# Kernel tuning notes

Measured on AMD Instinct MI355X. Metric: run time of the kernel, lower is better.

## Reference

```python
import jax, jax.numpy as jnp
import numpy as np

B, N, D_MODEL, LAP = 64, 64, 256, 16


def setup_inputs() -> dict:
    key = jax.random.key(0)
    ks = jax.random.split(key, 8)
    adj = jax.random.randint(ks[0], (B, N, N), 0, 2, dtype=jnp.int32)
    node_feats = jax.random.normal(ks[1], (B, N, D_MODEL), dtype=jnp.float32)
    eigvec = jax.random.normal(ks[2], (B, N, LAP), dtype=jnp.float32)
    W_lap = jax.random.normal(ks[3], (LAP, D_MODEL), dtype=jnp.float32) / np.sqrt(LAP)
    W_edge = jax.random.normal(ks[4], (1 + 2 * LAP, D_MODEL), dtype=jnp.float32) / np.sqrt(1 + 2 * LAP)
    b_edge = jax.random.normal(ks[5], (D_MODEL,), dtype=jnp.float32) * 0.02
    type_embed = jax.random.normal(ks[6], (2, D_MODEL), dtype=jnp.float32)
    graph_tok = jax.random.normal(ks[7], (1, 1, D_MODEL), dtype=jnp.float32)
    return {"adj": adj, "node_feats": node_feats, "eigvec": eigvec,
            "W_lap": W_lap, "W_edge": W_edge, "b_edge": b_edge,
            "type_embed": type_embed, "graph_tok": graph_tok}


def reference(adj, node_feats, eigvec, W_lap, W_edge, b_edge, type_embed, graph_tok):
    b, n, _ = adj.shape
    d = graph_tok.shape[-1]
    # node tokens: feats + LapPE projection
    node_tok = node_feats + jnp.einsum('bnl,ld->bnd', eigvec, W_lap)
    # upper-triangular candidate edges (fixed M = n(n-1)/2, jit-friendly)
    iu, ju = jnp.triu_indices(n, k=1)               # [M]
    valid = adj[:, iu, ju] > 0                       # [B, M]
    # stable compaction: valid edges first (matches torch per-graph extraction order)
    order = jnp.argsort(~valid, axis=1, stable=True) # [B, M]
    src = iu[order]                                  # [B, M]
    dst = ju[order]
    valid_sorted = jnp.take_along_axis(valid, order, axis=1)
    Pu = jnp.take_along_axis(eigvec, src[..., None], axis=1)  # [B, M, LAP]
    Pv = jnp.take_along_axis(eigvec, dst[..., None], axis=1)
    m = src.shape[1]
    edge_in = jnp.concatenate([jnp.ones((b, m, 1), eigvec.dtype), Pu, Pv], axis=-1)
    etok = jnp.einsum('bmf,fd->bmd', edge_in, W_edge) + b_edge + type_embed[1]
    etok = jnp.where(valid_sorted[..., None], etok, 0.0)      # zeros at padding
    pad_mask_edges = ~valid_sorted                             # True = padding
    gtok = jnp.broadcast_to(graph_tok, (b, 1, d))
    seq_embeds = jnp.concatenate([gtok, node_tok, etok], axis=1)  # [B, 1+n+M, d]
    pad_mask = jnp.concatenate([jnp.zeros((b, 1 + n), bool), pad_mask_edges], axis=1)
    return seq_embeds, pad_mask
```

## Files before the change

### kernel.cpp

```cpp
#include <hip/hip_runtime.h>

#define B_ 64
#define N_ 64
#define D_ 256
#define LAP_ 16
#define M_ 2016
#define TOK_ 2081

__global__ __launch_bounds__(256) void compact_kernel(const int* __restrict__ adj,
                                                      int* __restrict__ pack) {
    int b = blockIdx.x;
    int t = threadIdx.x;
    __shared__ int s[256];
    __shared__ int s_total;

    int ii[8], jj[8], vv[8];
    int c = 0;
#pragma unroll
    for (int k = 0; k < 8; k++) {
        int m = t * 8 + k;
        int valid = 0, i = 0, j = 0;
        if (m < M_) {
            float fm = (float)m;
            int gi = (int)((127.0f - sqrtf(127.0f * 127.0f - 8.0f * fm)) * 0.5f);
            if (gi < 0) gi = 0;
            if (gi > 62) gi = 62;
            while (gi > 0 && (127 * gi - gi * gi) / 2 > m) gi--;
            while (gi < 62 && (127 * (gi + 1) - (gi + 1) * (gi + 1)) / 2 <= m) gi++;
            i = gi;
            j = i + 1 + (m - (127 * i - i * i) / 2);
            valid = (adj[b * (N_ * N_) + i * N_ + j] > 0) ? 1 : 0;
        }
        ii[k] = i; jj[k] = j; vv[k] = valid;
        c += valid;
    }
    s[t] = c;
    __syncthreads();
    for (int off = 1; off < 256; off <<= 1) {
        int v = (t >= off) ? s[t - off] : 0;
        __syncthreads();
        s[t] += v;
        __syncthreads();
    }
    if (t == 255) s_total = s[255];
    __syncthreads();
    int total = s_total;
    int run = s[t] - c;
#pragma unroll
    for (int k = 0; k < 8; k++) {
        int m = t * 8 + k;
        if (m < M_) {
            int p;
            if (vv[k]) { p = run; run++; }
            else       { p = total + (m - run); }
            pack[b * M_ + p] = ii[k] | (jj[k] << 8) | (vv[k] << 16);
        }
    }
}

__global__ __launch_bounds__(256) void node_kernel(const float* __restrict__ node_feats,
                                                   const float* __restrict__ eigvec,
                                                   const float* __restrict__ W_lap,
                                                   const float* __restrict__ graph_tok,
                                                   float* __restrict__ out) {
    int b = blockIdx.x;
    int t = threadIdx.x;
    int n = blockIdx.y * 4 + (t >> 6);
    int lane = t & 63;
    const float* e = eigvec + (size_t)(b * N_ + n) * LAP_;
    float4 acc = ((const float4*)(node_feats + ((size_t)b * N_ + n) * D_))[lane];
#pragma unroll
    for (int l = 0; l < LAP_; l++) {
        float el = e[l];
        float4 w = ((const float4*)(W_lap + l * D_))[lane];
        acc.x += el * w.x; acc.y += el * w.y; acc.z += el * w.z; acc.w += el * w.w;
    }
    ((float4*)(out + (size_t)b * TOK_ * D_ + (size_t)(1 + n) * D_))[lane] = acc;

    if (blockIdx.y == 0) {
        out[(size_t)b * TOK_ * D_ + t] = graph_tok[t];
        float* mask = out + (size_t)B_ * TOK_ * D_;
        if (t < 1 + N_) mask[b * TOK_ + t] = 0.0f;
    }
}

__global__ __launch_bounds__(256) void edge_kernel(const float* __restrict__ eigvec,
                                                   const float* __restrict__ W_edge,
                                                   const float* __restrict__ b_edge,
                                                   const float* __restrict__ type_embed,
                                                   const int* __restrict__ pack,
                                                   float* __restrict__ out) {
    __shared__ float sEig[N_ * LAP_];

    int b = blockIdx.x;
    int t = threadIdx.x;
    int wave = t >> 6, lane = t & 63;

    ((float4*)sEig)[t] = ((const float4*)(eigvec + (size_t)b * N_ * LAP_))[t];

    float4 base = ((const float4*)W_edge)[lane];
    {
        float4 bb = ((const float4*)b_edge)[lane];
        float4 te = ((const float4*)(type_embed + D_))[lane];
        base.x += bb.x + te.x; base.y += bb.y + te.y;
        base.z += bb.z + te.z; base.w += bb.w + te.w;
    }
    float4 w1[LAP_], w2[LAP_];
#pragma unroll
    for (int l = 0; l < LAP_; l++) {
        w1[l] = ((const float4*)(W_edge + (1 + l) * D_))[lane];
        w2[l] = ((const float4*)(W_edge + (1 + LAP_ + l) * D_))[lane];
    }
    __syncthreads();

    float* maskb = out + (size_t)B_ * TOK_ * D_ + (size_t)b * TOK_ + 1 + N_;
    float* outb = out + (size_t)b * TOK_ * D_ + (size_t)(1 + N_) * D_;

#pragma unroll
    for (int k = 0; k < 8; k++) {
        int p = blockIdx.y * 32 + wave * 8 + k;
        int pk = pack[b * M_ + p];
        float4 acc = make_float4(0.f, 0.f, 0.f, 0.f);
        int valid = (pk >> 16) & 1;
        if (valid) {
            int si = pk & 0xff, di = (pk >> 8) & 0xff;
            const float4* eu4 = (const float4*)(sEig + si * LAP_);
            const float4* ev4 = (const float4*)(sEig + di * LAP_);
            float4 eu[4], ev[4];
#pragma unroll
            for (int q = 0; q < 4; q++) { eu[q] = eu4[q]; ev[q] = ev4[q]; }
            acc = base;
            const float* euf = (const float*)eu;
            const float* evf = (const float*)ev;
#pragma unroll
            for (int l = 0; l < LAP_; l++) {
                float pu = euf[l], pv = evf[l];
                acc.x += pu * w1[l].x + pv * w2[l].x;
                acc.y += pu * w1[l].y + pv * w2[l].y;
                acc.z += pu * w1[l].z + pv * w2[l].z;
                acc.w += pu * w1[l].w + pv * w2[l].w;
            }
        }
        ((float4*)(outb + (size_t)p * D_))[lane] = acc;
        if (lane == 0) maskb[p] = valid ? 0.0f : 1.0f;
    }
}

extern "C" void kernel_launch(void* const* d_in, const int* in_sizes, int n_in,
                              void* d_out, int out_size, void* d_ws, size_t ws_size,
                              hipStream_t stream) {
    const int*   adj        = (const int*)d_in[0];
    const float* node_feats = (const float*)d_in[1];
    const float* eigvec     = (const float*)d_in[2];
    const float* W_lap      = (const float*)d_in[3];
    const float* W_edge     = (const float*)d_in[4];
    const float* b_edge     = (const float*)d_in[5];
    const float* type_embed = (const float*)d_in[6];
    const float* graph_tok  = (const float*)d_in[7];
    float* out = (float*)d_out;
    int* pack = (int*)d_ws;

    compact_kernel<<<dim3(B_), dim3(256), 0, stream>>>(adj, pack);
    node_kernel<<<dim3(B_, 16), dim3(256), 0, stream>>>(node_feats, eigvec, W_lap,
                                                        graph_tok, out);
    edge_kernel<<<dim3(B_, 63), dim3(256), 0, stream>>>(eigvec, W_edge, b_edge,
                                                        type_embed, pack, out);
}
```

Baseline: 179.9 us.

## Fuse compaction, node and edge kernels into one launch with per-block ballot compaction

```diff
diff --git a/kernel.cpp b/kernel.cpp
--- a/kernel.cpp
+++ b/kernel.cpp
@@ -7,142 +7,171 @@
 #define M_ 2016
 #define TOK_ 2081
 
-__global__ __launch_bounds__(256) void compact_kernel(const int* __restrict__ adj,
-                                                      int* __restrict__ pack) {
-    int b = blockIdx.x;
-    int t = threadIdx.x;
-    __shared__ int s[256];
-    __shared__ int s_total;
+typedef float v4f __attribute__((ext_vector_type(4)));
+typedef float v2f __attribute__((ext_vector_type(2)));
 
-    int ii[8], jj[8], vv[8];
-    int c = 0;
-#pragma unroll
-    for (int k = 0; k < 8; k++) {
-        int m = t * 8 + k;
-        int valid = 0, i = 0, j = 0;
-        if (m < M_) {
-            float fm = (float)m;
-            int gi = (int)((127.0f - sqrtf(127.0f * 127.0f - 8.0f * fm)) * 0.5f);
-            if (gi < 0) gi = 0;
-            if (gi > 62) gi = 62;
-            while (gi > 0 && (127 * gi - gi * gi) / 2 > m) gi--;
-            while (gi < 62 && (127 * (gi + 1) - (gi + 1) * (gi + 1)) / 2 <= m) gi++;
-            i = gi;
-            j = i + 1 + (m - (127 * i - i * i) / 2);
-            valid = (adj[b * (N_ * N_) + i * N_ + j] > 0) ? 1 : 0;
-        }
-        ii[k] = i; jj[k] = j; vv[k] = valid;
-        c += valid;
-    }
-    s[t] = c;
-    __syncthreads();
-    for (int off = 1; off < 256; off <<= 1) {
-        int v = (t >= off) ? s[t - off] : 0;
-        __syncthreads();
-        s[t] += v;
-        __syncthreads();
-    }
-    if (t == 255) s_total = s[255];
-    __syncthreads();
-    int total = s_total;
-    int run = s[t] - c;
-#pragma unroll
-    for (int k = 0; k < 8; k++) {
-        int m = t * 8 + k;
-        if (m < M_) {
-            int p;
-            if (vv[k]) { p = run; run++; }
-            else       { p = total + (m - run); }
-            pack[b * M_ + p] = ii[k] | (jj[k] << 8) | (vv[k] << 16);
-        }
-    }
+__device__ __forceinline__ void ij_from_m(int m, int& i, int& j) {
+    float fm = (float)m;
+    int gi = (int)((127.0f - sqrtf(127.0f * 127.0f - 8.0f * fm)) * 0.5f);
+    if (gi < 0) gi = 0;
+    if (gi > 62) gi = 62;
+    while (gi > 0 && (127 * gi - gi * gi) / 2 > m) gi--;
+    while (gi < 62 && (127 * (gi + 1) - (gi + 1) * (gi + 1)) / 2 <= m) gi++;
+    i = gi;
+    j = gi + 1 + (m - (127 * gi - gi * gi) / 2);
 }
 
-__global__ __launch_bounds__(256) void node_kernel(const float* __restrict__ node_feats,
-                                                   const float* __restrict__ eigvec,
-                                                   const float* __restrict__ W_lap,
-                                                   const float* __restrict__ graph_tok,
-                                                   float* __restrict__ out) {
-    int b = blockIdx.x;
-    int t = threadIdx.x;
-    int n = blockIdx.y * 4 + (t >> 6);
-    int lane = t & 63;
-    const float* e = eigvec + (size_t)(b * N_ + n) * LAP_;
-    float4 acc = ((const float4*)(node_feats + ((size_t)b * N_ + n) * D_))[lane];
-#pragma unroll
-    for (int l = 0; l < LAP_; l++) {
-        float el = e[l];
-        float4 w = ((const float4*)(W_lap + l * D_))[lane];
-        acc.x += el * w.x; acc.y += el * w.y; acc.z += el * w.z; acc.w += el * w.w;
-    }
-    ((float4*)(out + (size_t)b * TOK_ * D_ + (size_t)(1 + n) * D_))[lane] = acc;
+__global__ __launch_bounds__(256, 4) void fused_kernel(
+    const int*   __restrict__ adj,
+    const float* __restrict__ node_feats,
+    const float* __restrict__ eigvec,
+    const float* __restrict__ W_lap,
+    const float* __restrict__ W_edge,
+    const float* __restrict__ b_edge,
+    const float* __restrict__ type_embed,
+    const float* __restrict__ graph_tok,
+    float*       __restrict__ out)
+{
+    __shared__ float sEig[N_ * LAP_];
+    __shared__ unsigned long long sWords[32];
+    __shared__ int sPref[32];
+    __shared__ int sTok[32];
+    __shared__ int sTotal;
 
-    if (blockIdx.y == 0) {
-        out[(size_t)b * TOK_ * D_ + t] = graph_tok[t];
-        float* mask = out + (size_t)B_ * TOK_ * D_;
-        if (t < 1 + N_) mask[b * TOK_ + t] = 0.0f;
-    }
-}
-
-__global__ __launch_bounds__(256) void edge_kernel(const float* __restrict__ eigvec,
-                                                   const float* __restrict__ W_edge,
-                                                   const float* __restrict__ b_edge,
-                                                   const float* __restrict__ type_embed,
-                                                   const int* __restrict__ pack,
-                                                   float* __restrict__ out) {
-    __shared__ float sEig[N_ * LAP_];
-
-    int b = blockIdx.x;
-    int t = threadIdx.x;
-    int wave = t >> 6, lane = t & 63;
+    const int b = blockIdx.x;
+    const int y = blockIdx.y;
+    const int t = threadIdx.x;
+    const int wave = t >> 6, lane = t & 63;
 
     ((float4*)sEig)[t] = ((const float4*)(eigvec + (size_t)b * N_ * LAP_))[t];
 
-    float4 base = ((const float4*)W_edge)[lane];
-    {
-        float4 bb = ((const float4*)b_edge)[lane];
-        float4 te = ((const float4*)(type_embed + D_))[lane];
-        base.x += bb.x + te.x; base.y += bb.y + te.y;
-        base.z += bb.z + te.z; base.w += bb.w + te.w;
+    if (y == 63) {
+        float4 wl[LAP_];
+#pragma unroll
+        for (int l = 0; l < LAP_; l++)
+            wl[l] = ((const float4*)(W_lap + l * D_))[lane];
+        __syncthreads();
+        float* outB = out + (size_t)b * TOK_ * D_;
+#pragma unroll 2
+        for (int it = 0; it < 16; it++) {
+            int n = it * 4 + wave;
+            float4 a = ((const float4*)(node_feats + ((size_t)b * N_ + n) * D_))[lane];
+            const float* e = sEig + n * LAP_;
+#pragma unroll
+            for (int l = 0; l < LAP_; l++) {
+                float el = e[l];
+                a.x += el * wl[l].x; a.y += el * wl[l].y;
+                a.z += el * wl[l].z; a.w += el * wl[l].w;
+            }
+            __builtin_nontemporal_store(*(const v4f*)&a,
+                (v4f*)(outB + (size_t)(1 + n) * D_) + lane);
+        }
+        outB[t] = graph_tok[t];
+        if (t < 1 + N_)
+            out[(size_t)B_ * TOK_ * D_ + (size_t)b * TOK_ + t] = 0.0f;
+        return;
     }
-    float4 w1[LAP_], w2[LAP_];
+
+#pragma unroll
+    for (int k = 0; k < 8; k++) {
+        int m = k * 256 + t;
+        int valid = 0;
+        if (m < M_) {
+            int i, j;
+            ij_from_m(m, i, j);
+            valid = (adj[b * (N_ * N_) + i * N_ + j] > 0) ? 1 : 0;
+        }
+        unsigned long long blt = __ballot(valid);
+        if (lane == 0) sWords[k * 4 + wave] = blt;
+    }
+
+    const int h = wave & 1;
+    const int cbase = h * 128 + lane * 2;
+    float2 base2;
+    base2.x = W_edge[cbase]     + b_edge[cbase]     + type_embed[D_ + cbase];
+    base2.y = W_edge[cbase + 1] + b_edge[cbase + 1] + type_embed[D_ + cbase + 1];
+    float2 w1[LAP_], w2[LAP_];
 #pragma unroll
     for (int l = 0; l < LAP_; l++) {
-        w1[l] = ((const float4*)(W_edge + (1 + l) * D_))[lane];
-        w2[l] = ((const float4*)(W_edge + (1 + LAP_ + l) * D_))[lane];
+        w1[l] = *(const float2*)(W_edge + (1 + l) * D_ + cbase);
+        w2[l] = *(const float2*)(W_edge + (1 + LAP_ + l) * D_ + cbase);
     }
     __syncthreads();
 
-    float* maskb = out + (size_t)B_ * TOK_ * D_ + (size_t)b * TOK_ + 1 + N_;
-    float* outb = out + (size_t)b * TOK_ * D_ + (size_t)(1 + N_) * D_;
+    if (t < 32) {
+        int c = __popcll(sWords[t]);
+        int inc = c;
+#pragma unroll
+        for (int off = 1; off < 32; off <<= 1) {
+            int v = __shfl_up(inc, off);
+            if (lane >= off) inc += v;
+        }
+        sPref[t] = inc - c;
+        if (t == 31) sTotal = inc;
+    }
+    __syncthreads();
 
-#pragma unroll
-    for (int k = 0; k < 8; k++) {
-        int p = blockIdx.y * 32 + wave * 8 + k;
-        int pk = pack[b * M_ + p];
-        float4 acc = make_float4(0.f, 0.f, 0.f, 0.f);
-        int valid = (pk >> 16) & 1;
-        if (valid) {
-            int si = pk & 0xff, di = (pk >> 8) & 0xff;
+    const int total = sTotal;
+    if (t < 32) {
+        int p = y * 32 + t;
+        int m, valid;
+        if (p < total) {
+            valid = 1;
+            int r = p;
+            int w = 0;
+            while (w < 31 && sPref[w + 1] <= r) w++;
+            unsigned long long x = sWords[w];
+            int rr = r - sPref[w];
+            for (int q = 0; q < rr; q++) x &= x - 1;
+            m = w * 64 + __builtin_ctzll(x);
+        } else {
+            valid = 0;
+            int r = p - total;
+            int w = 0;
+            while (w < 31 && (w + 1) * 64 - sPref[w + 1] <= r) w++;
+            unsigned long long x = ~sWords[w];
+            if (w == 31) x &= 0xFFFFFFFFull;
+            int rr = r - (w * 64 - sPref[w]);
+            for (int q = 0; q < rr; q++) x &= x - 1;
+            m = w * 64 + __builtin_ctzll(x);
+        }
+        int i, j;
+        ij_from_m(m, i, j);
+        sTok[t] = i | (j << 8) | (valid << 16);
+        out[(size_t)B_ * TOK_ * D_ + (size_t)b * TOK_ + 1 + N_ + p] =
+            valid ? 0.0f : 1.0f;
+    }
+    __syncthreads();
+
+    float* outE = out + (size_t)b * TOK_ * D_ + (size_t)(1 + N_) * D_;
+    const int tg = wave >> 1;
+#pragma unroll 2
+    for (int tt = 0; tt < 16; tt++) {
+        int slot = tg * 16 + tt;
+        int info = sTok[slot];
+        int p = y * 32 + slot;
+        float2 acc = make_float2(0.0f, 0.0f);
+        if (info >> 16) {
+            int si = info & 0xff, di = (info >> 8) & 0xff;
             const float4* eu4 = (const float4*)(sEig + si * LAP_);
             const float4* ev4 = (const float4*)(sEig + di * LAP_);
-            float4 eu[4], ev[4];
+            acc = base2;
 #pragma unroll
-            for (int q = 0; q < 4; q++) { eu[q] = eu4[q]; ev[q] = ev4[q]; }
-            acc = base;
-            const float* euf = (const float*)eu;
-            const float* evf = (const float*)ev;
-#pragma unroll
-            for (int l = 0; l < LAP_; l++) {
-                float pu = euf[l], pv = evf[l];
-                acc.x += pu * w1[l].x + pv * w2[l].x;
-                acc.y += pu * w1[l].y + pv * w2[l].y;
-                acc.z += pu * w1[l].z + pv * w2[l].z;
-                acc.w += pu * w1[l].w + pv * w2[l].w;
+            for (int q = 0; q < 4; q++) {
+                float4 u = eu4[q];
+                float4 v = ev4[q];
+                acc.x += u.x * w1[q*4+0].x + v.x * w2[q*4+0].x;
+                acc.y += u.x * w1[q*4+0].y + v.x * w2[q*4+0].y;
+                acc.x += u.y * w1[q*4+1].x + v.y * w2[q*4+1].x;
+                acc.y += u.y * w1[q*4+1].y + v.y * w2[q*4+1].y;
+                acc.x += u.z * w1[q*4+2].x + v.z * w2[q*4+2].x;
+                acc.y += u.z * w1[q*4+2].y + v.z * w2[q*4+2].y;
+                acc.x += u.w * w1[q*4+3].x + v.w * w2[q*4+3].x;
+                acc.y += u.w * w1[q*4+3].y + v.w * w2[q*4+3].y;
             }
         }
-        ((float4*)(outb + (size_t)p * D_))[lane] = acc;
-        if (lane == 0) maskb[p] = valid ? 0.0f : 1.0f;
+        __builtin_nontemporal_store(*(const v2f*)&acc,
+            (v2f*)(outE + (size_t)p * D_ + cbase));
     }
 }
 
@@ -158,11 +187,7 @@
     const float* type_embed = (const float*)d_in[6];
     const float* graph_tok  = (const float*)d_in[7];
     float* out = (float*)d_out;
-    int* pack = (int*)d_ws;
 
-    compact_kernel<<<dim3(B_), dim3(256), 0, stream>>>(adj, pack);
-    node_kernel<<<dim3(B_, 16), dim3(256), 0, stream>>>(node_feats, eigvec, W_lap,
-                                                        graph_tok, out);
-    edge_kernel<<<dim3(B_, 63), dim3(256), 0, stream>>>(eigvec, W_edge, b_edge,
-                                                        type_embed, pack, out);
+    fused_kernel<<<dim3(B_, 64), dim3(256), 0, stream>>>(
+        adj, node_feats, eigvec, W_lap, W_edge, b_edge, type_embed, graph_tok, out);
 }
```

New measurement: 209.1 us. 1.16x slower.
